# Optimization experiments

Hardware: AMD Instinct MI355X
Metric: run time of the kernel (lower is better)

The kernel has to match this reference:

```python
import jax, jax.numpy as jnp
import numpy as np

V = 100000
E = 524288
D_IN = 128
D_OUT = 128
NUM_REL = 474
BN_EPS = 1e-5


def setup_inputs() -> dict:
    key = jax.random.key(0)
    ks = jax.random.split(key, 12)
    return {
        "x": jax.random.normal(ks[0], (V, D_IN), dtype=jnp.float32),
        "rel_repr": jax.random.normal(ks[1], (NUM_REL, D_IN), dtype=jnp.float32),
        "edge_norm": jax.random.uniform(ks[2], (E,), dtype=jnp.float32),
        "in_w": jax.random.normal(ks[3], (D_IN, D_OUT), dtype=jnp.float32) * 0.1,
        "out_w": jax.random.normal(ks[4], (D_IN, D_OUT), dtype=jnp.float32) * 0.1,
        "loop_w": jax.random.normal(ks[5], (D_IN, D_OUT), dtype=jnp.float32) * 0.1,
        "w_rel": jax.random.normal(ks[6], (D_IN, D_OUT), dtype=jnp.float32) * 0.1,
        "loop_rel": jax.random.normal(ks[7], (1, D_IN), dtype=jnp.float32),
        "bias": jnp.zeros((D_OUT,), dtype=jnp.float32),
        "src": jax.random.randint(ks[8], (E,), 0, V, dtype=jnp.int32),
        "dst": jax.random.randint(ks[9], (E,), 0, V, dtype=jnp.int32),
        "edge_type": jax.random.randint(ks[10], (E,), 0, NUM_REL, dtype=jnp.int32),
    }


def reference(x, rel_repr, edge_norm, in_w, out_w, loop_w, w_rel, loop_rel, bias, src, dst, edge_type):
    # comp primitive 'mult': edge_data = src_emb * rel[edge_type]   [E, D_IN]
    rel = rel_repr  # num_base=-1 -> rel_wt is None, rel.data = rel_repr
    edge_data = x[src] * rel[edge_type]
    half = edge_data.shape[0] // 2  # static under jit
    # first half of edges -> in_w, second half -> out_w
    msg = jnp.concatenate([edge_data[:half] @ in_w, edge_data[half:] @ out_w], axis=0)
    msg = msg * edge_norm[:, None]
    # agg primitive 'sum': scatter-sum into dst nodes
    agg = jax.ops.segment_sum(msg, dst, num_segments=x.shape[0])  # [V, D_OUT]
    # self-loop path: comp(x, loop_rel) @ loop_w
    loop_msg = (x * loop_rel) @ loop_w
    # comb primitive 'add', scaled by 1/3 (dropout with p=0 is identity)
    h = (agg + loop_msg) * (1.0 / 3.0)
    h = h + bias
    # BatchNorm1d, training-mode batch stats, gamma=1, beta=0
    mean = jnp.mean(h, axis=0)
    var = jnp.mean((h - mean) ** 2, axis=0)
    h = (h - mean) * jax.lax.rsqrt(var + BN_EPS)
    # act primitive 'relu'; ltr=True -> project relations
    return jax.nn.relu(h), rel @ w_rel
```

## Files before the change

### kernel.cpp

```cpp
#include <hip/hip_runtime.h>

#define V 100000
#define VP 100096
#define E_EDGES 524288
#define HALF 262144
#define D 128
#define NREL 474
#define BN_EPS 1e-5f
#define NBLK 98

#define LDK 392
#define LDB 40

typedef unsigned short u16;
typedef unsigned int u32;
typedef unsigned long long u64;
typedef __attribute__((ext_vector_type(8))) short short8;
typedef __attribute__((ext_vector_type(4))) float f32x4;

__device__ __forceinline__ u16 f2bf(float f) {
    union { float f; u32 u; } v; v.f = f;
    u32 u = v.u;
    return (u16)((u + 0x7fffu + ((u >> 16) & 1u)) >> 16);
}
__device__ __forceinline__ u32 pk2(float a, float b) {
    return (u32)f2bf(a) | ((u32)f2bf(b) << 16);
}

__global__ __launch_bounds__(256) void hist_k(const int* __restrict__ dst, u32* __restrict__ cnt) {
    int e = blockIdx.x * 256 + threadIdx.x;
    if (e >= E_EDGES) return;
    u32 d = (u32)dst[e];
    if (d >= V) d = 0;
    atomicAdd(&cnt[d], 1u);
}

__global__ __launch_bounds__(1024) void scanA_k(const u32* __restrict__ cnt,
                                                u32* __restrict__ cursor,
                                                u32* __restrict__ bsum) {
    __shared__ u32 wsum[16];
    int tid = threadIdx.x, wid = tid >> 6, lane = tid & 63;
    int idx = blockIdx.x * 1024 + tid;
    u32 v = (idx < V) ? cnt[idx] : 0u;
    u32 s = v;
#pragma unroll
    for (int o = 1; o < 64; o <<= 1) {
        u32 t = __shfl_up(s, o, 64);
        if (lane >= o) s += t;
    }
    if (lane == 63) wsum[wid] = s;
    __syncthreads();
    if (wid == 0) {
        u32 wv = (lane < 16) ? wsum[lane] : 0u;
#pragma unroll
        for (int o = 1; o < 16; o <<= 1) {
            u32 t = __shfl_up(wv, o, 64);
            if (lane >= o) wv += t;
        }
        if (lane < 16) wsum[lane] = wv;
    }
    __syncthreads();
    u32 wprev = wid ? wsum[wid - 1] : 0u;
    if (idx < V) cursor[idx] = s + wprev - v;
    if (tid == 0) bsum[blockIdx.x] = wsum[15];
}

__global__ __launch_bounds__(128) void scanB_k(u32* __restrict__ bsum) {
    __shared__ u32 wtot;
    int t = threadIdx.x, lane = t & 63, w = t >> 6;
    u32 v = (t < NBLK) ? bsum[t] : 0u;
    u32 s = v;
#pragma unroll
    for (int o = 1; o < 64; o <<= 1) {
        u32 x = __shfl_up(s, o, 64);
        if (lane >= o) s += x;
    }
    if (w == 0 && lane == 63) wtot = s;
    __syncthreads();
    u32 add = (w == 1) ? wtot : 0u;
    if (t < NBLK) bsum[t] = add + s - v;
}

__global__ __launch_bounds__(1024) void scanC_k(u32* __restrict__ cursor,
                                                const u32* __restrict__ bsum) {
    int idx = blockIdx.x * 1024 + threadIdx.x;
    if (idx < V) cursor[idx] += bsum[blockIdx.x];
}

__global__ __launch_bounds__(256) void fill_rec_k(
    const int* __restrict__ dst, const int* __restrict__ src, const int* __restrict__ etype,
    const float* __restrict__ enorm, u32* __restrict__ cursor, u64* __restrict__ rec) {
    int e = blockIdx.x * 256 + threadIdx.x;
    if (e >= E_EDGES) return;
    u32 d = (u32)dst[e];   if (d >= V) d = 0;
    u32 s = (u32)src[e];   if (s >= V) s = 0;
    u32 t = (u32)etype[e]; if (t >= NREL) t = 0;
    float nm = enorm[e];
    u32 w = s | (t << 17) | ((e < HALF ? 0u : 1u) << 26);
    u32 slot = atomicAdd(&cursor[d], 1u);
    u64 r = (u64)w | ((u64)__float_as_uint(nm) << 32);
    if (slot < E_EDGES) rec[slot] = r;
}

struct Rec { u32 s, t, hf; float nm; };
__device__ __forceinline__ Rec dec(u64 r) {
    Rec q; u32 w = (u32)r;
    q.s = w & 0x1FFFFu;          if (q.s >= V) q.s = 0;
    q.t = (w >> 17) & 0x1FFu;    if (q.t >= NREL) q.t = 0;
    q.hf = (w >> 26) & 1u;
    q.nm = __uint_as_float((u32)(r >> 32));
    return q;
}

__global__ __launch_bounds__(256) void gather_k(
    const float* __restrict__ x, const float* __restrict__ rel,
    const u32* __restrict__ cursor, const u32* __restrict__ cnt,
    const u64* __restrict__ rec, u16* __restrict__ Aagg) {
    int wave = threadIdx.x >> 6, lane = threadIdx.x & 63;
    int v = blockIdx.x * 4 + wave;
    u32* arow = (u32*)(Aagg + (size_t)v * 256);
    if (v >= V) { arow[lane] = 0u; arow[64 + lane] = 0u; return; }

    u32 n = cnt[v], end = cursor[v];
    if (end > E_EDGES) end = E_EDGES;
    if (n > end) n = end;
    u32 p = end - n;
    int col = lane * 2;

    float iA0 = 0.f, iA1 = 0.f, oA0 = 0.f, oA1 = 0.f;
    float iB0 = 0.f, iB1 = 0.f, oB0 = 0.f, oB1 = 0.f;

    for (; p + 4 <= end; p += 4) {
        u64 r0 = rec[p], r1 = rec[p + 1], r2 = rec[p + 2], r3 = rec[p + 3];
        Rec q0 = dec(r0), q1 = dec(r1), q2 = dec(r2), q3 = dec(r3);
        float2 x0 = *(const float2*)(x + (size_t)q0.s * D + col);
        float2 x1 = *(const float2*)(x + (size_t)q1.s * D + col);
        float2 x2 = *(const float2*)(x + (size_t)q2.s * D + col);
        float2 x3 = *(const float2*)(x + (size_t)q3.s * D + col);
        float2 v0 = *(const float2*)(rel + (size_t)q0.t * D + col);
        float2 v1 = *(const float2*)(rel + (size_t)q1.t * D + col);
        float2 v2 = *(const float2*)(rel + (size_t)q2.t * D + col);
        float2 v3 = *(const float2*)(rel + (size_t)q3.t * D + col);
        float f00 = x0.x * v0.x * q0.nm, f01 = x0.y * v0.y * q0.nm;
        float f10 = x1.x * v1.x * q1.nm, f11 = x1.y * v1.y * q1.nm;
        float f20 = x2.x * v2.x * q2.nm, f21 = x2.y * v2.y * q2.nm;
        float f30 = x3.x * v3.x * q3.nm, f31 = x3.y * v3.y * q3.nm;
        if (q0.hf) { oA0 += f00; oA1 += f01; } else { iA0 += f00; iA1 += f01; }
        if (q1.hf) { oB0 += f10; oB1 += f11; } else { iB0 += f10; iB1 += f11; }
        if (q2.hf) { oA0 += f20; oA1 += f21; } else { iA0 += f20; iA1 += f21; }
        if (q3.hf) { oB0 += f30; oB1 += f31; } else { iB0 += f30; iB1 += f31; }
    }
    for (; p < end; p++) {
        u64 r0 = rec[p];
        Rec q0 = dec(r0);
        float2 x0 = *(const float2*)(x + (size_t)q0.s * D + col);
        float2 v0 = *(const float2*)(rel + (size_t)q0.t * D + col);
        float f00 = x0.x * v0.x * q0.nm, f01 = x0.y * v0.y * q0.nm;
        if (q0.hf) { oA0 += f00; oA1 += f01; } else { iA0 += f00; iA1 += f01; }
    }
    float a0 = iA0 + iB0, a1 = iA1 + iB1;
    float b0 = oA0 + oB0, b1 = oA1 + oB1;
    arow[lane]      = pk2(a0, a1);
    arow[64 + lane] = pk2(b0, b1);
}

__global__ __launch_bounds__(128) void bt_k(
    const float* __restrict__ in_w, const float* __restrict__ out_w,
    const float* __restrict__ loop_w, u16* __restrict__ Bt) {
    int n = blockIdx.x;
    int t = threadIdx.x;
    const float* Ws[3] = {in_w, out_w, loop_w};
#pragma unroll
    for (int seg = 0; seg < 3; seg++)
        Bt[(size_t)n * 384 + seg * 128 + t] = f2bf(Ws[seg][(size_t)t * D + n]);
}

__global__ __launch_bounds__(256) void gemm_k(
    const u16* __restrict__ Aagg, const u16* __restrict__ Bt,
    const float* __restrict__ x, const float* __restrict__ loop_rel,
    float* __restrict__ h_out, float* __restrict__ colsum, float* __restrict__ colsumsq) {
    __shared__ float s_sum[D], s_sq[D];
    int tid = threadIdx.x, wave = tid >> 6, lane = tid & 63;
    int row0 = blockIdx.x * 64;
    if (tid < D) { s_sum[tid] = 0.f; s_sq[tid] = 0.f; }
    __syncthreads();

    int m = wave * 16 + (lane & 15);
    int kq = (lane >> 4) * 8;
    int gvm = row0 + m;
    const u16* arow = Aagg + (size_t)(row0 + m) * 256;

    f32x4 acc[8];
#pragma unroll
    for (int ct = 0; ct < 8; ct++) acc[ct] = (f32x4){0.f, 0.f, 0.f, 0.f};

#pragma unroll
    for (int ks = 0; ks < 8; ks++) {
        short8 a = *(const short8*)(arow + ks * 32 + kq);
#pragma unroll
        for (int ct = 0; ct < 8; ct++) {
            short8 b = *(const short8*)(Bt + (size_t)(ct * 16 + (lane & 15)) * 384 + ks * 32 + kq);
            acc[ct] = __builtin_amdgcn_mfma_f32_16x16x32_bf16(a, b, acc[ct], 0, 0, 0);
        }
    }
#pragma unroll
    for (int kk = 0; kk < 4; kk++) {
        short8 a = (short8){0, 0, 0, 0, 0, 0, 0, 0};
        if (gvm < V) {
            const float* xp = x + (size_t)gvm * D + kk * 32 + kq;
            const float* lp = loop_rel + kk * 32 + kq;
            float4 x0 = *(const float4*)xp, x1 = *(const float4*)(xp + 4);
            float4 l0 = *(const float4*)lp, l1 = *(const float4*)(lp + 4);
            union { u32 u[4]; short8 s; } c;
            c.u[0] = pk2(x0.x * l0.x, x0.y * l0.y);
            c.u[1] = pk2(x0.z * l0.z, x0.w * l0.w);
            c.u[2] = pk2(x1.x * l1.x, x1.y * l1.y);
            c.u[3] = pk2(x1.z * l1.z, x1.w * l1.w);
            a = c.s;
        }
#pragma unroll
        for (int ct = 0; ct < 8; ct++) {
            short8 b = *(const short8*)(Bt + (size_t)(ct * 16 + (lane & 15)) * 384 + 256 + kk * 32 + kq);
            acc[ct] = __builtin_amdgcn_mfma_f32_16x16x32_bf16(a, b, acc[ct], 0, 0, 0);
        }
    }

    int m4 = (lane >> 4) * 4;
#pragma unroll
    for (int ct = 0; ct < 8; ct++) {
        float ls = 0.f, lq = 0.f;
#pragma unroll
        for (int i = 0; i < 4; i++) {
            int gv = row0 + wave * 16 + m4 + i;
            if (gv < V) {
                float h = acc[ct][i] * (1.0f / 3.0f);
                h_out[(size_t)gv * D + ct * 16 + (lane & 15)] = h;
                ls += h; lq += h * h;
            }
        }
        atomicAdd(&s_sum[ct * 16 + (lane & 15)], ls);
        atomicAdd(&s_sq[ct * 16 + (lane & 15)], lq);
    }
    __syncthreads();
    if (tid < D) atomicAdd(&colsum[tid], s_sum[tid]);
    else atomicAdd(&colsumsq[tid - D], s_sq[tid - D]);
}

__global__ void bn_finalize(const float* __restrict__ colsum, const float* __restrict__ colsumsq,
                            float* __restrict__ mean, float* __restrict__ scale) {
    int t = threadIdx.x;
    float m = colsum[t] * (1.0f / (float)V);
    if (!isfinite(m)) m = 0.f;
    float var = colsumsq[t] * (1.0f / (float)V) - m * m;
    if (!isfinite(var) || var < 0.f) var = 0.f;
    mean[t] = m;
    scale[t] = rsqrtf(var + BN_EPS);
}

__global__ __launch_bounds__(256) void bn_relu(
    float* __restrict__ hio, const float* __restrict__ mean, const float* __restrict__ scale) {
    int idx = (blockIdx.x * 256 + threadIdx.x) * 4;
    if (idx >= V * D) return;
    int col = idx & (D - 1);
    float4 hv = *(const float4*)(hio + idx);
    float f0 = (hv.x - mean[col + 0]) * scale[col + 0];
    float f1 = (hv.y - mean[col + 1]) * scale[col + 1];
    float f2 = (hv.z - mean[col + 2]) * scale[col + 2];
    float f3 = (hv.w - mean[col + 3]) * scale[col + 3];
    f0 = (f0 > 0.f) ? f0 : 0.f;
    f1 = (f1 > 0.f) ? f1 : 0.f;
    f2 = (f2 > 0.f) ? f2 : 0.f;
    f3 = (f3 > 0.f) ? f3 : 0.f;
    float4 ov; ov.x = f0; ov.y = f1; ov.z = f2; ov.w = f3;
    *(float4*)(hio + idx) = ov;
}

__global__ __launch_bounds__(128) void rel_gemm(
    const float* __restrict__ rel, const float* __restrict__ w, float* __restrict__ out1) {
    __shared__ float rs[D];
    int t = threadIdx.x;
    int r = blockIdx.x;
    rs[t] = rel[(size_t)r * D + t];
    __syncthreads();
    float s = 0.f;
#pragma unroll 8
    for (int k = 0; k < D; k++) s += rs[k] * w[(size_t)k * D + t];
    out1[(size_t)r * D + t] = s;
}

__global__ __launch_bounds__(1024) void scan_k(const u32* __restrict__ cnt,
                                               u32* __restrict__ cursor) {
    __shared__ u32 wsum[16];
    __shared__ u32 carry_s;
    int tid = threadIdx.x, wid = tid >> 6, lane = tid & 63;
    if (tid == 0) carry_s = 0;
    __syncthreads();
    for (int base = 0; base < V; base += 1024) {
        int idx = base + tid;
        u32 v = (idx < V) ? cnt[idx] : 0u;
        u32 s = v;
#pragma unroll
        for (int o = 1; o < 64; o <<= 1) {
            u32 t = __shfl_up(s, o, 64);
            if (lane >= o) s += t;
        }
        if (lane == 63) wsum[wid] = s;
        __syncthreads();
        if (wid == 0) {
            u32 wv = (lane < 16) ? wsum[lane] : 0u;
#pragma unroll
            for (int o = 1; o < 16; o <<= 1) {
                u32 t = __shfl_up(wv, o, 64);
                if (lane >= o) wv += t;
            }
            if (lane < 16) wsum[lane] = wv;
        }
        __syncthreads();
        u32 wprev = (wid == 0) ? 0u : wsum[wid - 1];
        u32 c = carry_s;
        if (idx < V) cursor[idx] = c + s + wprev - v;
        u32 tot = wsum[15];
        __syncthreads();
        if (tid == 0) carry_s = c + tot;
        __syncthreads();
    }
}

__global__ __launch_bounds__(256) void fill_k(
    const int* __restrict__ dst, u32* __restrict__ cursor, u32* __restrict__ eid) {
    int e = blockIdx.x * 256 + threadIdx.x;
    if (e >= E_EDGES) return;
    u32 d = (u32)dst[e];
    if (d >= V) d = 0;
    u32 slot = atomicAdd(&cursor[d], 1u);
    if (slot < E_EDGES) eid[slot] = (u32)e;
}

__global__ __launch_bounds__(256, 1) void fused_k(
    const float* __restrict__ x, const float* __restrict__ rel, const float* __restrict__ loop_rel,
    const float* __restrict__ in_w, const float* __restrict__ out_w, const float* __restrict__ loop_w,
    const float* __restrict__ enorm,
    const int* __restrict__ src, const int* __restrict__ etype,
    const u32* __restrict__ cursor, const u32* __restrict__ cnt,
    const u32* __restrict__ eid,
    float* __restrict__ h_out, float* __restrict__ colsum, float* __restrict__ colsumsq) {
    __shared__ u16 Alds[64 * LDK];
    __shared__ u16 Bs[D * LDB];
    __shared__ float s_sum[D], s_sq[D];

    int tid = threadIdx.x, wave = tid >> 6, lane = tid & 63;
    int row0 = blockIdx.x * 64;

    if (tid < D) { s_sum[tid] = 0.f; s_sq[tid] = 0.f; }

    for (int i = 0; i < 16; i++) {
        int row = wave * 16 + i;
        int gv = row0 + row;
        u32* arow = (u32*)(Alds + row * LDK);
        if (gv < V) {
            float a0 = 0.f, a1 = 0.f, b0 = 0.f, b1 = 0.f;
            float c0 = 0.f, c1 = 0.f, d0 = 0.f, d1 = 0.f;
            u32 n = cnt[gv];
            u32 end = cursor[gv];
            u32 beg = (end >= n) ? end - n : 0u;
            if (beg >= E_EDGES) { beg = 0; n = 0; }
            if (n > E_EDGES - beg) n = E_EDGES - beg;
            u32 nend = beg + n;
            u32 p = beg;
            for (; p + 2 <= nend; p += 2) {
                u32 e0 = eid[p];           if (e0 >= E_EDGES) e0 = 0;
                u32 e1 = eid[p + 1];       if (e1 >= E_EDGES) e1 = 0;
                u32 s0 = (u32)src[e0];     if (s0 >= V) s0 = 0;
                u32 s1 = (u32)src[e1];     if (s1 >= V) s1 = 0;
                u32 t0 = (u32)etype[e0];   if (t0 >= NREL) t0 = 0;
                u32 t1 = (u32)etype[e1];   if (t1 >= NREL) t1 = 0;
                float n0 = enorm[e0];
                float n1 = enorm[e1];
                float2 xv0 = *(const float2*)(x + (size_t)s0 * D + lane * 2);
                float2 xv1 = *(const float2*)(x + (size_t)s1 * D + lane * 2);
                float2 rv0 = *(const float2*)(rel + (size_t)t0 * D + lane * 2);
                float2 rv1 = *(const float2*)(rel + (size_t)t1 * D + lane * 2);
                float f00 = xv0.x * rv0.x * n0, f01 = xv0.y * rv0.y * n0;
                float f10 = xv1.x * rv1.x * n1, f11 = xv1.y * rv1.y * n1;
                if (e0 < HALF) { a0 += f00; a1 += f01; } else { b0 += f00; b1 += f01; }
                if (e1 < HALF) { c0 += f10; c1 += f11; } else { d0 += f10; d1 += f11; }
            }
            if (p < nend) {
                u32 e0 = eid[p];           if (e0 >= E_EDGES) e0 = 0;
                u32 s0 = (u32)src[e0];     if (s0 >= V) s0 = 0;
                u32 t0 = (u32)etype[e0];   if (t0 >= NREL) t0 = 0;
                float n0 = enorm[e0];
                float2 xv0 = *(const float2*)(x + (size_t)s0 * D + lane * 2);
                float2 rv0 = *(const float2*)(rel + (size_t)t0 * D + lane * 2);
                float f00 = xv0.x * rv0.x * n0, f01 = xv0.y * rv0.y * n0;
                if (e0 < HALF) { a0 += f00; a1 += f01; } else { b0 += f00; b1 += f01; }
            }
            a0 += c0; a1 += c1; b0 += d0; b1 += d1;
            float2 xv = *(const float2*)(x + (size_t)gv * D + lane * 2);
            float2 lv = *(const float2*)(loop_rel + lane * 2);
            arow[lane]       = pk2(a0, a1);
            arow[64 + lane]  = pk2(b0, b1);
            arow[128 + lane] = pk2(xv.x * lv.x, xv.y * lv.y);
        } else {
            arow[lane] = 0u; arow[64 + lane] = 0u; arow[128 + lane] = 0u;
        }
    }
    __syncthreads();

    f32x4 acc[8];
#pragma unroll
    for (int ct = 0; ct < 8; ct++) acc[ct] = (f32x4){0.f, 0.f, 0.f, 0.f};

    int m = wave * 16 + (lane & 15);
    int kq = (lane >> 4) * 8;
    int bk = tid >> 3;
    int bn0 = (tid & 7) * 16;

    for (int ks = 0; ks < 12; ks++) {
        int k0 = ks * 32;
        int seg = k0 >> 7;
        int kloc = k0 & 127;
        const float* W = (seg == 0) ? in_w : (seg == 1 ? out_w : loop_w);
#pragma unroll
        for (int j = 0; j < 16; j += 2) {
            float2 w2 = *(const float2*)(W + (size_t)(kloc + bk) * D + bn0 + j);
            Bs[(bn0 + j) * LDB + bk]     = f2bf(w2.x);
            Bs[(bn0 + j + 1) * LDB + bk] = f2bf(w2.y);
        }
        __syncthreads();
        short8 a = *(const short8*)(Alds + m * LDK + k0 + kq);
#pragma unroll
        for (int ct = 0; ct < 8; ct++) {
            short8 b = *(const short8*)(Bs + (ct * 16 + (lane & 15)) * LDB + kq);
            acc[ct] = __builtin_amdgcn_mfma_f32_16x16x32_bf16(a, b, acc[ct], 0, 0, 0);
        }
        __syncthreads();
    }

    int m4 = (lane >> 4) * 4;
#pragma unroll
    for (int ct = 0; ct < 8; ct++) {
        float ls = 0.f, lq = 0.f;
#pragma unroll
        for (int i = 0; i < 4; i++) {
            int gv = row0 + wave * 16 + m4 + i;
            if (gv < V) {
                float h = acc[ct][i] * (1.0f / 3.0f);
                h_out[(size_t)gv * D + ct * 16 + (lane & 15)] = h;
                ls += h; lq += h * h;
            }
        }
        atomicAdd(&s_sum[ct * 16 + (lane & 15)], ls);
        atomicAdd(&s_sq[ct * 16 + (lane & 15)], lq);
    }
    __syncthreads();
    if (tid < D) atomicAdd(&colsum[tid], s_sum[tid]);
    else atomicAdd(&colsumsq[tid - D], s_sq[tid - D]);
}

extern "C" void kernel_launch(void* const* d_in, const int* in_sizes, int n_in,
                              void* d_out, int out_size, void* d_ws, size_t ws_size,
                              hipStream_t stream) {
    const float* x        = (const float*)d_in[0];
    const float* rel_repr = (const float*)d_in[1];
    const float* enorm    = (const float*)d_in[2];
    const float* in_w     = (const float*)d_in[3];
    const float* out_w    = (const float*)d_in[4];
    const float* loop_w   = (const float*)d_in[5];
    const float* w_rel    = (const float*)d_in[6];
    const float* loop_rel = (const float*)d_in[7];
    const int* src   = (const int*)d_in[9];
    const int* dst   = (const int*)d_in[10];
    const int* etype = (const int*)d_in[11];

    float* out0 = (float*)d_out;
    float* out1 = (float*)d_out + (size_t)V * D;

    char* ws = (char*)d_ws;

    {
        size_t off = 0;
        u32* cnt        = (u32*)(ws + off); off += (size_t)V * 4;
        float* colsum   = (float*)(ws + off); off += 512;
        float* colsumsq = (float*)(ws + off); off += 512;
        size_t zero_bytes = off;
        u32* cursor = (u32*)(ws + off); off += (size_t)V * 4;
        float* meanp  = (float*)(ws + off); off += 512;
        float* scalep = (float*)(ws + off); off += 512;
        u32* bsum   = (u32*)(ws + off); off += 512;
        u16* Bt     = (u16*)(ws + off); off += (size_t)384 * 128 * 2;
        u64* rec    = (u64*)(ws + off); off += (size_t)E_EDGES * 8;
        u16* Aagg   = (u16*)(ws + off); off += (size_t)VP * 256 * 2;

        if (ws_size >= off) {
            hipMemsetAsync(d_ws, 0, zero_bytes, stream);
            bt_k<<<128, 128, 0, stream>>>(in_w, out_w, loop_w, Bt);
            hist_k<<<(E_EDGES + 255) / 256, 256, 0, stream>>>(dst, cnt);
            scanA_k<<<NBLK, 1024, 0, stream>>>(cnt, cursor, bsum);
            scanB_k<<<1, 128, 0, stream>>>(bsum);
            scanC_k<<<NBLK, 1024, 0, stream>>>(cursor, bsum);
            fill_rec_k<<<(E_EDGES + 255) / 256, 256, 0, stream>>>(dst, src, etype, enorm, cursor, rec);
            gather_k<<<VP / 4, 256, 0, stream>>>(x, rel_repr, cursor, cnt, rec, Aagg);
            gemm_k<<<VP / 64, 256, 0, stream>>>(Aagg, Bt, x, loop_rel, out0, colsum, colsumsq);
            bn_finalize<<<1, 128, 0, stream>>>(colsum, colsumsq, meanp, scalep);
            bn_relu<<<(V * D / 4 + 255) / 256, 256, 0, stream>>>(out0, meanp, scalep);
            rel_gemm<<<NREL, 128, 0, stream>>>(rel_repr, w_rel, out1);
            return;
        }
    }

    {
        size_t off = 0;
        u32* cnt      = (u32*)(ws + off); off += (size_t)V * 4;
        float* colsum = (float*)(ws + off); off += 512;
        float* colsumsq = (float*)(ws + off); off += 512;
        size_t zero_bytes = off;
        u32* cursor   = (u32*)(ws + off); off += (size_t)V * 4;
        float* meanp  = (float*)(ws + off); off += 512;
        float* scalep = (float*)(ws + off); off += 512;
        u32* eid      = (u32*)(ws + off); off += (size_t)E_EDGES * 4;

        if (ws_size < off) return;

        hipMemsetAsync(d_ws, 0, zero_bytes, stream);
        hist_k<<<(E_EDGES + 255) / 256, 256, 0, stream>>>(dst, cnt);
        scan_k<<<1, 1024, 0, stream>>>(cnt, cursor);
        fill_k<<<(E_EDGES + 255) / 256, 256, 0, stream>>>(dst, cursor, eid);
        fused_k<<<(V + 63) / 64, 256, 0, stream>>>(x, rel_repr, loop_rel, in_w, out_w, loop_w,
                                                   enorm, src, etype,
                                                   cursor, cnt, eid,
                                                   out0, colsum, colsumsq);
        bn_finalize<<<1, 128, 0, stream>>>(colsum, colsumsq, meanp, scalep);
        bn_relu<<<(V * D / 4 + 255) / 256, 256, 0, stream>>>(out0, meanp, scalep);
        rel_gemm<<<NREL, 128, 0, stream>>>(rel_repr, w_rel, out1);
    }
}
```

Baseline: 388.3 us.

## Stage weight tile in LDS, split GEMM columns across blocks, two-level BN reduction

The node GEMM now copies a padded 64-column half of the transposed bf16 weight matrix into shared memory and reads B fragments from there instead of global memory. Each block covers 128 rows and 64 output columns with 512 threads. Per-block column sums are written to a partial buffer and reduced by a new kernel, which replaces the per-block global atomics. This cuts repeated global B loads and atomic contention. In exchange it adds an LDS fill per block, an extra kernel launch and re-reads of the A rows by both column halves.

```diff
diff --git a/kernel.cpp b/kernel.cpp
--- a/kernel.cpp
+++ b/kernel.cpp
@@ -8,6 +8,10 @@
 #define NREL 474
 #define BN_EPS 1e-5f
 #define NBLK 98
+
+#define BTP 392
+#define ROWTILES 782
+#define RED_BLKS 98
 
 #define LDK 392
 #define LDB 40
@@ -172,34 +176,49 @@
     const float* Ws[3] = {in_w, out_w, loop_w};
 #pragma unroll
     for (int seg = 0; seg < 3; seg++)
-        Bt[(size_t)n * 384 + seg * 128 + t] = f2bf(Ws[seg][(size_t)t * D + n]);
-}
-
-__global__ __launch_bounds__(256) void gemm_k(
+        Bt[(size_t)n * BTP + seg * 128 + t] = f2bf(Ws[seg][(size_t)t * D + n]);
+    if (t < BTP - 384) Bt[(size_t)n * BTP + 384 + t] = 0;
+}
+
+__global__ __launch_bounds__(512, 4) void gemm_k(
     const u16* __restrict__ Aagg, const u16* __restrict__ Bt,
     const float* __restrict__ x, const float* __restrict__ loop_rel,
-    float* __restrict__ h_out, float* __restrict__ colsum, float* __restrict__ colsumsq) {
-    __shared__ float s_sum[D], s_sq[D];
+    float* __restrict__ h_out, float* __restrict__ psum, float* __restrict__ psq) {
+    __shared__ u16 Bs[64 * BTP];
+    __shared__ float s_sum[64], s_sq[64];
     int tid = threadIdx.x, wave = tid >> 6, lane = tid & 63;
-    int row0 = blockIdx.x * 64;
-    if (tid < D) { s_sum[tid] = 0.f; s_sq[tid] = 0.f; }
-    __syncthreads();
-
-    int m = wave * 16 + (lane & 15);
+    int half = blockIdx.x & 1;
+    int rt   = blockIdx.x >> 1;
+    int row0 = rt * 128;
+
+    if (tid < 64) s_sum[tid] = 0.f;
+    else if (tid < 128) s_sq[tid - 64] = 0.f;
+
+    {
+        const u16* srcB = Bt + (size_t)half * 64 * BTP;
+#pragma unroll
+        for (int it = 0; it < 7; it++) {
+            int c = it * 512 + tid;
+            if (c < 3136) *(short8*)(Bs + (size_t)c * 8) = *(const short8*)(srcB + (size_t)c * 8);
+        }
+    }
+    __syncthreads();
+
+    int m16 = lane & 15;
     int kq = (lane >> 4) * 8;
-    int gvm = row0 + m;
-    const u16* arow = Aagg + (size_t)(row0 + m) * 256;
-
-    f32x4 acc[8];
-#pragma unroll
-    for (int ct = 0; ct < 8; ct++) acc[ct] = (f32x4){0.f, 0.f, 0.f, 0.f};
+    int gvm = row0 + wave * 16 + m16;
+    const u16* arow = Aagg + (size_t)gvm * 256;
+
+    f32x4 acc[4];
+#pragma unroll
+    for (int ct = 0; ct < 4; ct++) acc[ct] = (f32x4){0.f, 0.f, 0.f, 0.f};
 
 #pragma unroll
     for (int ks = 0; ks < 8; ks++) {
         short8 a = *(const short8*)(arow + ks * 32 + kq);
 #pragma unroll
-        for (int ct = 0; ct < 8; ct++) {
-            short8 b = *(const short8*)(Bt + (size_t)(ct * 16 + (lane & 15)) * 384 + ks * 32 + kq);
+        for (int ct = 0; ct < 4; ct++) {
+            short8 b = *(const short8*)(Bs + (size_t)(ct * 16 + m16) * BTP + ks * 32 + kq);
             acc[ct] = __builtin_amdgcn_mfma_f32_16x16x32_bf16(a, b, acc[ct], 0, 0, 0);
         }
     }
@@ -219,31 +238,47 @@
             a = c.s;
         }
 #pragma unroll
-        for (int ct = 0; ct < 8; ct++) {
-            short8 b = *(const short8*)(Bt + (size_t)(ct * 16 + (lane & 15)) * 384 + 256 + kk * 32 + kq);
+        for (int ct = 0; ct < 4; ct++) {
+            short8 b = *(const short8*)(Bs + (size_t)(ct * 16 + m16) * BTP + 256 + kk * 32 + kq);
             acc[ct] = __builtin_amdgcn_mfma_f32_16x16x32_bf16(a, b, acc[ct], 0, 0, 0);
         }
     }
 
     int m4 = (lane >> 4) * 4;
 #pragma unroll
-    for (int ct = 0; ct < 8; ct++) {
+    for (int ct = 0; ct < 4; ct++) {
         float ls = 0.f, lq = 0.f;
 #pragma unroll
         for (int i = 0; i < 4; i++) {
             int gv = row0 + wave * 16 + m4 + i;
             if (gv < V) {
                 float h = acc[ct][i] * (1.0f / 3.0f);
-                h_out[(size_t)gv * D + ct * 16 + (lane & 15)] = h;
+                h_out[(size_t)gv * D + half * 64 + ct * 16 + m16] = h;
                 ls += h; lq += h * h;
             }
         }
-        atomicAdd(&s_sum[ct * 16 + (lane & 15)], ls);
-        atomicAdd(&s_sq[ct * 16 + (lane & 15)], lq);
-    }
-    __syncthreads();
-    if (tid < D) atomicAdd(&colsum[tid], s_sum[tid]);
-    else atomicAdd(&colsumsq[tid - D], s_sq[tid - D]);
+        atomicAdd(&s_sum[ct * 16 + m16], ls);
+        atomicAdd(&s_sq[ct * 16 + m16], lq);
+    }
+    __syncthreads();
+    if (tid < 64) psum[(size_t)rt * 128 + half * 64 + tid] = s_sum[tid];
+    else if (tid < 128) psq[(size_t)rt * 128 + half * 64 + (tid - 64)] = s_sq[tid - 64];
+}
+
+__global__ __launch_bounds__(256) void bn_reduce(
+    const float* __restrict__ psum, const float* __restrict__ psq,
+    float* __restrict__ colsum, float* __restrict__ colsumsq) {
+    int t = threadIdx.x;
+    int c = t & 127;
+    const float* srcp = (t < 128) ? psum : psq;
+    float s = 0.f;
+    int r0 = blockIdx.x * 8;
+#pragma unroll
+    for (int i = 0; i < 8; i++) {
+        int r = r0 + i;
+        if (r < ROWTILES) s += srcp[(size_t)r * 128 + c];
+    }
+    atomicAdd(((t < 128) ? colsum : colsumsq) + c, s);
 }
 
 __global__ void bn_finalize(const float* __restrict__ colsum, const float* __restrict__ colsumsq,
@@ -488,7 +523,9 @@
         float* meanp  = (float*)(ws + off); off += 512;
         float* scalep = (float*)(ws + off); off += 512;
         u32* bsum   = (u32*)(ws + off); off += 512;
-        u16* Bt     = (u16*)(ws + off); off += (size_t)384 * 128 * 2;
+        u16* Bt     = (u16*)(ws + off); off += (size_t)128 * BTP * 2;
+        float* psum = (float*)(ws + off); off += (size_t)ROWTILES * 128 * 4;
+        float* psq  = (float*)(ws + off); off += (size_t)ROWTILES * 128 * 4;
         u64* rec    = (u64*)(ws + off); off += (size_t)E_EDGES * 8;
         u16* Aagg   = (u16*)(ws + off); off += (size_t)VP * 256 * 2;
 
@@ -501,7 +538,8 @@
             scanC_k<<<NBLK, 1024, 0, stream>>>(cursor, bsum);
             fill_rec_k<<<(E_EDGES + 255) / 256, 256, 0, stream>>>(dst, src, etype, enorm, cursor, rec);
             gather_k<<<VP / 4, 256, 0, stream>>>(x, rel_repr, cursor, cnt, rec, Aagg);
-            gemm_k<<<VP / 64, 256, 0, stream>>>(Aagg, Bt, x, loop_rel, out0, colsum, colsumsq);
+            gemm_k<<<ROWTILES * 2, 512, 0, stream>>>(Aagg, Bt, x, loop_rel, out0, psum, psq);
+            bn_reduce<<<RED_BLKS, 256, 0, stream>>>(psum, psq, colsum, colsumsq);
             bn_finalize<<<1, 128, 0, stream>>>(colsum, colsumsq, meanp, scalep);
             bn_relu<<<(V * D / 4 + 255) / 256, 256, 0, stream>>>(out0, meanp, scalep);
             rel_gemm<<<NREL, 128, 0, stream>>>(rel_repr, w_rel, out1);
```

New measurement: 332.7 us. 1.17x faster.
